# Kernel tuning notes

Measured on AMD Instinct MI355X. Metric: run time of the kernel, lower is better.

Reference implementation:

```python
import jax, jax.numpy as jnp
import numpy as np

B, DIM_IN, DIM_OUT = 2048, 4096, 4096


def setup_inputs() -> dict:
    key = jax.random.key(0)
    k1, k2, k3 = jax.random.split(key, 3)
    # binary input activations (0/1), stored as int32
    x = jax.random.randint(k1, (B, DIM_IN), 0, 2, dtype=jnp.int32)
    masks = jax.random.uniform(k2, (DIM_IN, DIM_OUT)) < 0.5
    # integer thresholds in [0, dim_in)
    thresholds = jax.random.randint(k3, (DIM_OUT,), 0, DIM_IN, dtype=jnp.int32)
    return {"x": x, "masks": masks, "thresholds": thresholds}


def reference(x, masks, thresholds):
    # Original: expand x to (B, dim_in, dim_out), XNOR with masks, sum over dim_in,
    # compare vs thresholds. XNOR(a,b) = a*b + (1-a)*(1-b), so the sum over dim_in
    # is two GEMMs -- never materialize the (B, dim_in, dim_out) tensor.
    xf = x.astype(jnp.float32)              # (B, dim_in), values in {0,1}
    mf = masks.astype(jnp.float32)          # (dim_in, dim_out)
    sums = xf @ mf + (1.0 - xf) @ (1.0 - mf)  # (B, dim_out), popcount of agreements
    return sums > thresholds.astype(jnp.float32)[None, :]  # (B, dim_out) bool
```

## Files before the change

kernel.cpp:

```cpp
#include <hip/hip_runtime.h>
#include <stdint.h>

#define BB    2048
#define DIN   4096
#define DOUT  4096


using v4i  = __attribute__((ext_vector_type(4)))  int;
using v16i = __attribute__((ext_vector_type(16))) int;

__device__ __forceinline__ void async_load16(const void* g, void* l) {
    __builtin_amdgcn_global_load_lds(
        (const __attribute__((address_space(1))) unsigned int*)g,
        (__attribute__((address_space(3))) unsigned int*)l,
        16, 0, 0);
}

__device__ __forceinline__ unsigned int to_pm1(unsigned int c) {
    return c + ((c ^ 0x01010101u) * 255u);
}

__global__ void pack_all(const int* __restrict__ x,
                         const void* __restrict__ mraw,
                         char* __restrict__ x8,
                         char* __restrict__ m8T) {
    const int tid = threadIdx.x;
    if (blockIdx.x < BB) {
        const int row = blockIdx.x;
        const int4* src = (const int4*)(x + (size_t)row * DIN);
        unsigned int* dst = (unsigned int*)(x8 + (size_t)row * DIN);
        #pragma unroll
        for (int q = 0; q < 4; ++q) {
            int4 v = src[q * 256 + tid];
            unsigned int t = (unsigned int)(v.x & 1) |
                             ((unsigned int)(v.y & 1) << 8) |
                             ((unsigned int)(v.z & 1) << 16) |
                             ((unsigned int)(v.w & 1) << 24);
            dst[q * 256 + tid] = to_pm1(t);
        }
    } else {
        const int bw = blockIdx.x - BB;
        const int k0 = (bw & 63) * 64;
        const int n0 = (bw >> 6) * 64;

        const unsigned char* mb = (const unsigned char*)mraw;
        int myv = (mb[tid] != 0) + (mb[tid + 256] != 0) +
                  (mb[tid + 512] != 0) + (mb[tid + 768] != 0);
        #pragma unroll
        for (int d = 32; d; d >>= 1) myv += __shfl_xor(myv, d);
        const bool isU8 = (myv > 64);

        const int n4 = (tid & 15) * 4;
        const int k4 = (tid >> 4) * 4;
        unsigned int a[4];
        if (isU8) {
            #pragma unroll
            for (int r = 0; r < 4; ++r)
                a[r] = *(const unsigned int*)(mb + (size_t)(k0 + k4 + r) * DOUT + n0 + n4);
        } else {
            const int4* m32 = (const int4*)mraw;
            #pragma unroll
            for (int r = 0; r < 4; ++r) {
                int4 v = m32[((size_t)(k0 + k4 + r) * DOUT + n0 + n4) >> 2];
                a[r] = (unsigned int)(v.x & 1) |
                       ((unsigned int)(v.y & 1) << 8) |
                       ((unsigned int)(v.z & 1) << 16) |
                       ((unsigned int)(v.w & 1) << 24);
            }
        }
        unsigned int x0 = __builtin_amdgcn_perm(a[1], a[0], 0x05010400u);
        unsigned int x1 = __builtin_amdgcn_perm(a[3], a[2], 0x05010400u);
        unsigned int x2 = __builtin_amdgcn_perm(a[1], a[0], 0x07030602u);
        unsigned int x3 = __builtin_amdgcn_perm(a[3], a[2], 0x07030602u);
        unsigned int c0 = __builtin_amdgcn_perm(x1, x0, 0x05040100u);
        unsigned int c1 = __builtin_amdgcn_perm(x1, x0, 0x07060302u);
        unsigned int c2 = __builtin_amdgcn_perm(x3, x2, 0x05040100u);
        unsigned int c3 = __builtin_amdgcn_perm(x3, x2, 0x07060302u);
        *(unsigned int*)(m8T + (size_t)(n0 + n4 + 0) * DIN + k0 + k4) = to_pm1(c0);
        *(unsigned int*)(m8T + (size_t)(n0 + n4 + 1) * DIN + k0 + k4) = to_pm1(c1);
        *(unsigned int*)(m8T + (size_t)(n0 + n4 + 2) * DIN + k0 + k4) = to_pm1(c2);
        *(unsigned int*)(m8T + (size_t)(n0 + n4 + 3) * DIN + k0 + k4) = to_pm1(c3);
    }
}

__global__ __launch_bounds__(256)
void bgemm(const char* __restrict__ x8,
           const char* __restrict__ m8T,
           const int* __restrict__ thr,
           int* __restrict__ out) {
    const int flat = blockIdx.y * 32 + blockIdx.x;
    const int xcd  = flat & 7;
    const int idx  = flat >> 3;
    const int bm   = (xcd & 1) * 8 + (idx & 7);
    const int bn   = (xcd >> 1) * 8 + (idx >> 3);
    const int b0   = bm * 128;
    const int o0   = bn * 128;

    const int tid  = threadIdx.x;
    const int lane = tid & 63;
    const int wv   = tid >> 6;
    const int wm   = (wv & 1) * 64;
    const int wn   = (wv >> 1) * 64;
    const int l31  = lane & 31;
    const int lh   = lane >> 5;
    const int rsw  = l31 & 7;

    __shared__ __align__(16) char lA[2][128 * 128];
    __shared__ __align__(16) char lB[2][128 * 128];

    auto stage = [&](int c, int buf) {
        const int k0  = c * 128;
        const int r8  = lane >> 3;
        const int s   = lane & 7;
        #pragma unroll
        for (int h = 0; h < 4; ++h) {
            const int r0  = wv * 32 + h * 8;
            const int row = r0 + r8;
            const int g   = s ^ (row & 7);
            async_load16(x8 + (size_t)(b0 + row) * DIN + k0 + g * 16,
                         &lA[buf][r0 * 128 + lane * 16]);
            async_load16(m8T + (size_t)(o0 + row) * DIN + k0 + g * 16,
                         &lB[buf][r0 * 128 + lane * 16]);
        }
    };

    v16i acc[2][2];
    #pragma unroll
    for (int t = 0; t < 2; ++t)
        #pragma unroll
        for (int u = 0; u < 2; ++u)
            acc[t][u] = (v16i)(0);

    stage(0, 0);
    __syncthreads();

    for (int c = 0; c < 32; ++c) {
        const int buf = c & 1;
        if (c < 31) stage(c + 1, buf ^ 1);

        #pragma unroll
        for (int ks = 0; ks < 4; ++ks) {
            const int slot = ((ks * 2 + lh) ^ rsw) * 16;
            v4i aF[2], bF[2];
            #pragma unroll
            for (int t = 0; t < 2; ++t) {
                aF[t] = *(const v4i*)&lA[buf][(wm + t * 32 + l31) * 128 + slot];
                bF[t] = *(const v4i*)&lB[buf][(wn + t * 32 + l31) * 128 + slot];
            }
            acc[0][0] = __builtin_amdgcn_mfma_i32_32x32x32_i8(aF[0], bF[0], acc[0][0], 0, 0, 0);
            acc[0][1] = __builtin_amdgcn_mfma_i32_32x32x32_i8(aF[0], bF[1], acc[0][1], 0, 0, 0);
            acc[1][0] = __builtin_amdgcn_mfma_i32_32x32x32_i8(aF[1], bF[0], acc[1][0], 0, 0, 0);
            acc[1][1] = __builtin_amdgcn_mfma_i32_32x32x32_i8(aF[1], bF[1], acc[1][1], 0, 0, 0);
        }
        __syncthreads();
    }

    #pragma unroll
    for (int u = 0; u < 2; ++u) {
        const int o   = o0 + wn + u * 32 + l31;
        const int lim = 2 * thr[o] - DIN;
        #pragma unroll
        for (int t = 0; t < 2; ++t) {
            #pragma unroll
            for (int r = 0; r < 16; ++r) {
                const int rowl = (r & 3) + 8 * (r >> 2) + 4 * lh;
                const int b    = b0 + wm + t * 32 + rowl;
                out[(size_t)b * DOUT + o] = (acc[t][u][r] > lim) ? 1 : 0;
            }
        }
    }
}

extern "C" void kernel_launch(void* const* d_in, const int* in_sizes, int n_in,
                              void* d_out, int out_size, void* d_ws, size_t ws_size,
                              hipStream_t stream) {
    const int* x          = (const int*)d_in[0];
    const void* masks     = d_in[1];
    const int* thresholds = (const int*)d_in[2];
    int* out              = (int*)d_out;

    char* x8  = (char*)d_ws;
    char* m8T = (char*)d_ws + ((size_t)8 << 20);

    pack_all<<<BB + 4096, 256, 0, stream>>>(x, masks, x8, m8T);
    bgemm<<<dim3(32, 16), 256, 0, stream>>>(x8, m8T, thresholds, out);
}
```

Baseline: 176.9 us.

## Enlarge bgemm block tile to 256x128 with one block per CU

Each block now computes a 256x128 output tile with 4 waves each owning 64x128, so B fragments are shared across all waves and global/LDS traffic per MFMA drops. The grid halves to 256 blocks, matching the CU count, and launch bounds request one block per CU. In exchange, occupancy falls, accumulator register pressure doubles, LDS use grows to 96 KB, and the inner loop unroll is reduced.

```diff
diff --git a/kernel.cpp b/kernel.cpp
--- a/kernel.cpp
+++ b/kernel.cpp
@@ -83,7 +83,7 @@
     }
 }
 
-__global__ __launch_bounds__(256)
+__global__ __launch_bounds__(256, 1)
 void bgemm(const char* __restrict__ x8,
            const char* __restrict__ m8T,
            const int* __restrict__ thr,
@@ -91,44 +91,49 @@
     const int flat = blockIdx.y * 32 + blockIdx.x;
     const int xcd  = flat & 7;
     const int idx  = flat >> 3;
-    const int bm   = (xcd & 1) * 8 + (idx & 7);
-    const int bn   = (xcd >> 1) * 8 + (idx >> 3);
-    const int b0   = bm * 128;
+    const int bm   = (xcd & 1) * 4 + (idx & 3);
+    const int bn   = (xcd >> 1) * 8 + (idx >> 2);
+    const int m0   = bm * 256;
     const int o0   = bn * 128;
 
     const int tid  = threadIdx.x;
     const int lane = tid & 63;
     const int wv   = tid >> 6;
-    const int wm   = (wv & 1) * 64;
-    const int wn   = (wv >> 1) * 64;
+    const int wm   = wv * 64;
     const int l31  = lane & 31;
     const int lh   = lane >> 5;
     const int rsw  = l31 & 7;
 
-    __shared__ __align__(16) char lA[2][128 * 128];
+    __shared__ __align__(16) char lA[2][256 * 128];
     __shared__ __align__(16) char lB[2][128 * 128];
 
     auto stage = [&](int c, int buf) {
-        const int k0  = c * 128;
-        const int r8  = lane >> 3;
-        const int s   = lane & 7;
+        const int k0 = c * 128;
+        const int r8 = lane >> 3;
+        const int s  = lane & 7;
+        #pragma unroll
+        for (int h = 0; h < 8; ++h) {
+            const int r0  = wv * 64 + h * 8;
+            const int row = r0 + r8;
+            const int g   = s ^ (row & 7);
+            async_load16(x8 + (size_t)(m0 + row) * DIN + k0 + g * 16,
+                         &lA[buf][r0 * 128 + lane * 16]);
+        }
         #pragma unroll
         for (int h = 0; h < 4; ++h) {
             const int r0  = wv * 32 + h * 8;
             const int row = r0 + r8;
             const int g   = s ^ (row & 7);
-            async_load16(x8 + (size_t)(b0 + row) * DIN + k0 + g * 16,
-                         &lA[buf][r0 * 128 + lane * 16]);
             async_load16(m8T + (size_t)(o0 + row) * DIN + k0 + g * 16,
                          &lB[buf][r0 * 128 + lane * 16]);
         }
     };
 
-    v16i acc[2][2];
+    v16i acc[2][4];
     #pragma unroll
     for (int t = 0; t < 2; ++t)
         #pragma unroll
-        for (int u = 0; u < 2; ++u)
+        for (int u = 0; u < 4; ++u)
             acc[t][u] = (v16i)(0);
 
     stage(0, 0);
@@ -138,33 +143,36 @@
         const int buf = c & 1;
         if (c < 31) stage(c + 1, buf ^ 1);
 
-        #pragma unroll
+        #pragma unroll 2
         for (int ks = 0; ks < 4; ++ks) {
             const int slot = ((ks * 2 + lh) ^ rsw) * 16;
-            v4i aF[2], bF[2];
+            v4i aF[2], bF[4];
             #pragma unroll
-            for (int t = 0; t < 2; ++t) {
+            for (int t = 0; t < 2; ++t)
                 aF[t] = *(const v4i*)&lA[buf][(wm + t * 32 + l31) * 128 + slot];
-                bF[t] = *(const v4i*)&lB[buf][(wn + t * 32 + l31) * 128 + slot];
-            }
-            acc[0][0] = __builtin_amdgcn_mfma_i32_32x32x32_i8(aF[0], bF[0], acc[0][0], 0, 0, 0);
-            acc[0][1] = __builtin_amdgcn_mfma_i32_32x32x32_i8(aF[0], bF[1], acc[0][1], 0, 0, 0);
-            acc[1][0] = __builtin_amdgcn_mfma_i32_32x32x32_i8(aF[1], bF[0], acc[1][0], 0, 0, 0);
-            acc[1][1] = __builtin_amdgcn_mfma_i32_32x32x32_i8(aF[1], bF[1], acc[1][1], 0, 0, 0);
+            #pragma unroll
+            for (int u = 0; u < 4; ++u)
+                bF[u] = *(const v4i*)&lB[buf][(u * 32 + l31) * 128 + slot];
+            #pragma unroll
+            for (int t = 0; t < 2; ++t)
+                #pragma unroll
+                for (int u = 0; u < 4; ++u)
+                    acc[t][u] = __builtin_amdgcn_mfma_i32_32x32x32_i8(
+                        aF[t], bF[u], acc[t][u], 0, 0, 0);
         }
         __syncthreads();
     }
 
     #pragma unroll
-    for (int u = 0; u < 2; ++u) {
-        const int o   = o0 + wn + u * 32 + l31;
+    for (int u = 0; u < 4; ++u) {
+        const int o   = o0 + u * 32 + l31;
         const int lim = 2 * thr[o] - DIN;
         #pragma unroll
         for (int t = 0; t < 2; ++t) {
             #pragma unroll
             for (int r = 0; r < 16; ++r) {
                 const int rowl = (r & 3) + 8 * (r >> 2) + 4 * lh;
-                const int b    = b0 + wm + t * 32 + rowl;
+                const int b    = m0 + wm + t * 32 + rowl;
                 out[(size_t)b * DOUT + o] = (acc[t][u][r] > lim) ? 1 : 0;
             }
         }
@@ -183,5 +191,5 @@
     char* m8T = (char*)d_ws + ((size_t)8 << 20);
 
     pack_all<<<BB + 4096, 256, 0, stream>>>(x, masks, x8, m8T);
-    bgemm<<<dim3(32, 16), 256, 0, stream>>>(x8, m8T, thresholds, out);
+    bgemm<<<dim3(32, 8), 256, 0, stream>>>(x8, m8T, thresholds, out);
 }
```

Result: slower. 186.3 us (+5.3%).

## Repack operands into k-panel-major 16-byte layout for contiguous GEMM staging

Applied to the files above, without the earlier changes.

Changes the packed int8 layouts of x and the transposed masks so that each 16-element k-slice of all rows is stored contiguously (panel-major), rather than row-major across the full K dimension. The GEMM staging loads now read fully contiguous 2KB or 4KB runs per panel, and the LDS layout becomes panel-major without the XOR swizzle. The x pack kernel is restructured so each thread handles one row and writes 16-byte panel entries. This trades possible LDS bank conflicts on the fragment reads (now a stride of 16 bytes across lanes) and strided input reads in the pack step for better global coalescing in the main loop.

```diff
diff --git a/kernel.cpp b/kernel.cpp
--- a/kernel.cpp
+++ b/kernel.cpp
@@ -22,24 +22,32 @@
 
 __global__ void pack_all(const int* __restrict__ x,
                          const void* __restrict__ mraw,
-                         char* __restrict__ x8,
-                         char* __restrict__ m8T) {
+                         char* __restrict__ x8p,
+                         char* __restrict__ b8p) {
     const int tid = threadIdx.x;
-    if (blockIdx.x < BB) {
-        const int row = blockIdx.x;
-        const int4* src = (const int4*)(x + (size_t)row * DIN);
-        unsigned int* dst = (unsigned int*)(x8 + (size_t)row * DIN);
+    if (blockIdx.x < 256) {
+        const int br  = blockIdx.x & 31;
+        const int bp  = blockIdx.x >> 5;
+        const int row = br * 64 + (tid & 63);
+        const int w   = tid >> 6;
         #pragma unroll
-        for (int q = 0; q < 4; ++q) {
-            int4 v = src[q * 256 + tid];
-            unsigned int t = (unsigned int)(v.x & 1) |
-                             ((unsigned int)(v.y & 1) << 8) |
-                             ((unsigned int)(v.z & 1) << 16) |
-                             ((unsigned int)(v.w & 1) << 24);
-            dst[q * 256 + tid] = to_pm1(t);
+        for (int j = 0; j < 8; ++j) {
+            const int p = bp * 32 + w * 8 + j;
+            const int4* src = (const int4*)(x + (size_t)row * DIN + p * 16);
+            int4 a0 = src[0], a1 = src[1], a2 = src[2], a3 = src[3];
+            uint4 v;
+            v.x = to_pm1((unsigned)(a0.x & 1) | ((unsigned)(a0.y & 1) << 8) |
+                         ((unsigned)(a0.z & 1) << 16) | ((unsigned)(a0.w & 1) << 24));
+            v.y = to_pm1((unsigned)(a1.x & 1) | ((unsigned)(a1.y & 1) << 8) |
+                         ((unsigned)(a1.z & 1) << 16) | ((unsigned)(a1.w & 1) << 24));
+            v.z = to_pm1((unsigned)(a2.x & 1) | ((unsigned)(a2.y & 1) << 8) |
+                         ((unsigned)(a2.z & 1) << 16) | ((unsigned)(a2.w & 1) << 24));
+            v.w = to_pm1((unsigned)(a3.x & 1) | ((unsigned)(a3.y & 1) << 8) |
+                         ((unsigned)(a3.z & 1) << 16) | ((unsigned)(a3.w & 1) << 24));
+            *(uint4*)(x8p + ((size_t)p * 2048 + row) * 16) = v;
         }
     } else {
-        const int bw = blockIdx.x - BB;
+        const int bw = blockIdx.x - 256;
         const int k0 = (bw & 63) * 64;
         const int n0 = (bw >> 6) * 64;
 
@@ -76,16 +84,18 @@
         unsigned int c1 = __builtin_amdgcn_perm(x1, x0, 0x07060302u);
         unsigned int c2 = __builtin_amdgcn_perm(x3, x2, 0x05040100u);
         unsigned int c3 = __builtin_amdgcn_perm(x3, x2, 0x07060302u);
-        *(unsigned int*)(m8T + (size_t)(n0 + n4 + 0) * DIN + k0 + k4) = to_pm1(c0);
-        *(unsigned int*)(m8T + (size_t)(n0 + n4 + 1) * DIN + k0 + k4) = to_pm1(c1);
-        *(unsigned int*)(m8T + (size_t)(n0 + n4 + 2) * DIN + k0 + k4) = to_pm1(c2);
-        *(unsigned int*)(m8T + (size_t)(n0 + n4 + 3) * DIN + k0 + k4) = to_pm1(c3);
+        const int p   = (k0 + k4) >> 4;
+        const int off = k4 & 15;
+        *(unsigned int*)(b8p + ((size_t)p * 4096 + n0 + n4 + 0) * 16 + off) = to_pm1(c0);
+        *(unsigned int*)(b8p + ((size_t)p * 4096 + n0 + n4 + 1) * 16 + off) = to_pm1(c1);
+        *(unsigned int*)(b8p + ((size_t)p * 4096 + n0 + n4 + 2) * 16 + off) = to_pm1(c2);
+        *(unsigned int*)(b8p + ((size_t)p * 4096 + n0 + n4 + 3) * 16 + off) = to_pm1(c3);
     }
 }
 
 __global__ __launch_bounds__(256)
-void bgemm(const char* __restrict__ x8,
-           const char* __restrict__ m8T,
+void bgemm(const char* __restrict__ x8p,
+           const char* __restrict__ b8p,
            const int* __restrict__ thr,
            int* __restrict__ out) {
     const int flat = blockIdx.y * 32 + blockIdx.x;
@@ -93,7 +103,7 @@
     const int idx  = flat >> 3;
     const int bm   = (xcd & 1) * 8 + (idx & 7);
     const int bn   = (xcd >> 1) * 8 + (idx >> 3);
-    const int b0   = bm * 128;
+    const int m0   = bm * 128;
     const int o0   = bn * 128;
 
     const int tid  = threadIdx.x;
@@ -103,24 +113,23 @@
     const int wn   = (wv >> 1) * 64;
     const int l31  = lane & 31;
     const int lh   = lane >> 5;
-    const int rsw  = l31 & 7;
 
-    __shared__ __align__(16) char lA[2][128 * 128];
-    __shared__ __align__(16) char lB[2][128 * 128];
+    __shared__ __align__(16) char lA[2][8 * 128 * 16];
+    __shared__ __align__(16) char lB[2][8 * 128 * 16];
 
     auto stage = [&](int c, int buf) {
-        const int k0  = c * 128;
-        const int r8  = lane >> 3;
-        const int s   = lane & 7;
         #pragma unroll
-        for (int h = 0; h < 4; ++h) {
-            const int r0  = wv * 32 + h * 8;
-            const int row = r0 + r8;
-            const int g   = s ^ (row & 7);
-            async_load16(x8 + (size_t)(b0 + row) * DIN + k0 + g * 16,
-                         &lA[buf][r0 * 128 + lane * 16]);
-            async_load16(m8T + (size_t)(o0 + row) * DIN + k0 + g * 16,
-                         &lB[buf][r0 * 128 + lane * 16]);
+        for (int pp = 0; pp < 2; ++pp) {
+            const int pl = 2 * wv + pp;
+            const int pg = 8 * c + pl;
+            #pragma unroll
+            for (int h = 0; h < 2; ++h) {
+                const int r = h * 64 + lane;
+                async_load16(x8p + ((size_t)pg * 2048 + m0 + r) * 16,
+                             &lA[buf][(pl * 128 + r) * 16]);
+                async_load16(b8p + ((size_t)pg * 4096 + o0 + r) * 16,
+                             &lB[buf][(pl * 128 + r) * 16]);
+            }
         }
     };
 
@@ -140,12 +149,12 @@
 
         #pragma unroll
         for (int ks = 0; ks < 4; ++ks) {
-            const int slot = ((ks * 2 + lh) ^ rsw) * 16;
+            const int poff = (2 * ks + lh) * 2048;
             v4i aF[2], bF[2];
             #pragma unroll
             for (int t = 0; t < 2; ++t) {
-                aF[t] = *(const v4i*)&lA[buf][(wm + t * 32 + l31) * 128 + slot];
-                bF[t] = *(const v4i*)&lB[buf][(wn + t * 32 + l31) * 128 + slot];
+                aF[t] = *(const v4i*)&lA[buf][poff + (wm + t * 32 + l31) * 16];
+                bF[t] = *(const v4i*)&lB[buf][poff + (wn + t * 32 + l31) * 16];
             }
             acc[0][0] = __builtin_amdgcn_mfma_i32_32x32x32_i8(aF[0], bF[0], acc[0][0], 0, 0, 0);
             acc[0][1] = __builtin_amdgcn_mfma_i32_32x32x32_i8(aF[0], bF[1], acc[0][1], 0, 0, 0);
@@ -164,7 +173,7 @@
             #pragma unroll
             for (int r = 0; r < 16; ++r) {
                 const int rowl = (r & 3) + 8 * (r >> 2) + 4 * lh;
-                const int b    = b0 + wm + t * 32 + rowl;
+                const int b    = m0 + wm + t * 32 + rowl;
                 out[(size_t)b * DOUT + o] = (acc[t][u][r] > lim) ? 1 : 0;
             }
         }
@@ -179,9 +188,9 @@
     const int* thresholds = (const int*)d_in[2];
     int* out              = (int*)d_out;
 
-    char* x8  = (char*)d_ws;
-    char* m8T = (char*)d_ws + ((size_t)8 << 20);
+    char* x8p = (char*)d_ws;
+    char* b8p = (char*)d_ws + ((size_t)8 << 20);
 
-    pack_all<<<BB + 4096, 256, 0, stream>>>(x, masks, x8, m8T);
-    bgemm<<<dim3(32, 16), 256, 0, stream>>>(x8, m8T, thresholds, out);
+    pack_all<<<256 + 4096, 256, 0, stream>>>(x, masks, x8p, b8p);
+    bgemm<<<dim3(32, 16), 256, 0, stream>>>(x8p, b8p, thresholds, out);
 }
```

Measured after the change: 177.9 us. About the same (+0.6%).
